# Kernel optimization log

Measured on AMD Instinct MI355X. Metric: run time of the kernel, lower is better.

## Reference

```python
import jax, jax.numpy as jnp
import numpy as np

N_NODES = 50000
N_EDGES = 800000
D = 128
DEPTH = 3


def setup_inputs() -> dict:
    key = jax.random.key(0)
    ks = jax.random.split(key, 10)
    s = 1.0 / np.sqrt(D)
    return {
        "h": jax.random.normal(ks[0], (N_NODES, D), dtype=jnp.float32),
        "src": jax.random.randint(ks[1], (N_EDGES,), 0, N_NODES, dtype=jnp.int32),
        "dst": jax.random.randint(ks[2], (N_EDGES,), 0, N_NODES, dtype=jnp.int32),
        "W_in1": jax.random.normal(ks[3], (D, D), dtype=jnp.float32) * s,
        "b_in1": jnp.zeros((D,), dtype=jnp.float32),
        "W_in2": jax.random.normal(ks[4], (D, D), dtype=jnp.float32) * s,
        "b_in2": jnp.zeros((D,), dtype=jnp.float32),
        "W_self": jax.random.normal(ks[5], (DEPTH, D, D), dtype=jnp.float32) * s,
        "b_self": jnp.zeros((DEPTH, D), dtype=jnp.float32),
        "W_neigh": jax.random.normal(ks[6], (DEPTH, D, D), dtype=jnp.float32) * s,
    }


def _mean_aggregate(h, src, dst, n_nodes):
    # gather source features along edges, sum into destination, divide by in-degree
    msg = h[src]                                             # [E, D]
    summed = jax.ops.segment_sum(msg, dst, num_segments=n_nodes)  # [N, D]
    deg = jax.ops.segment_sum(jnp.ones_like(dst, dtype=h.dtype), dst,
                              num_segments=n_nodes)          # [N]
    return summed / jnp.maximum(deg, 1.0)[:, None]


def reference(h, src, dst, W_in1, b_in1, W_in2, b_in2, W_self, b_self, W_neigh):
    n_nodes = h.shape[0]
    # fc_in: Linear -> tanh -> Linear
    h = jnp.tanh(h @ W_in1 + b_in1) @ W_in2 + b_in2
    # stacked SAGEConv(mean) layers with SiLU between layers
    for i in range(DEPTH):
        h_neigh = _mean_aggregate(h, src, dst, n_nodes)
        h = h @ W_self[i] + b_self[i] + h_neigh @ W_neigh[i]
        if i < DEPTH - 1:
            h = jax.nn.silu(h)
    return jnp.tanh(h)
```

## Files before the change

kernel.cpp:

```cpp
#include <hip/hip_runtime.h>
#include <stdint.h>

#define DD 128
#define LDSROW 136

typedef __attribute__((ext_vector_type(8))) short short8;
typedef __attribute__((ext_vector_type(4))) float float4v;

__device__ __forceinline__ unsigned short f2bf(float f) {
  unsigned u = __float_as_uint(f);
  unsigned r = u + 0x7fffu + ((u >> 16) & 1u);
  return (unsigned short)(r >> 16);
}
__device__ __forceinline__ unsigned pack2(float a, float b) {
  return (unsigned)f2bf(a) | ((unsigned)f2bf(b) << 16);
}
__device__ __forceinline__ float2 unpack2(unsigned p) {
  float2 r;
  r.x = __uint_as_float(p << 16);
  r.y = __uint_as_float(p & 0xffff0000u);
  return r;
}

__global__ __launch_bounds__(256) void k_deg_prep(const int* __restrict__ dst, int* deg, int e, int eb,
                                                  const float* __restrict__ W1, const float* __restrict__ W2,
                                                  const float* __restrict__ Wself, const float* __restrict__ Wneigh,
                                                  unsigned* __restrict__ wfrag) {
  int b = blockIdx.x;
  if (b < eb) {
    int i = b * 256 + threadIdx.x;
    if (i < e) atomicAdd(&deg[dst[i]], 1);
  } else {
    int gid = (b - eb) * 256 + threadIdx.x;
    int m = gid >> 13;
    int r = gid & 8191;
    int p = r & 3;
    int lane = (r >> 2) & 63;
    int t = (r >> 8) & 3;
    int c = r >> 10;
    const float* W;
    if (m == 0) W = W1;
    else if (m == 1) W = W2;
    else if (m < 5) W = Wself + (size_t)(m - 2) * DD * DD;
    else W = Wneigh + (size_t)(m - 5) * DD * DD;
    int n = c * 16 + (lane & 15);
    int k = t * 32 + (lane >> 4) * 8 + 2 * p;
    wfrag[gid] = pack2(W[(size_t)k * DD + n], W[(size_t)(k + 1) * DD + n]);
  }
}

__global__ __launch_bounds__(1024) void k_scan1(const int* __restrict__ deg, int* __restrict__ incl,
                                                int* __restrict__ bsum, int n) {
  __shared__ int sh[1024];
  int t = threadIdx.x;
  int i = blockIdx.x * 1024 + t;
  int v = (i < n) ? deg[i] : 0;
  sh[t] = v;
  __syncthreads();
#pragma unroll
  for (int off = 1; off < 1024; off <<= 1) {
    int add = (t >= off) ? sh[t - off] : 0;
    __syncthreads();
    sh[t] += add;
    __syncthreads();
  }
  if (i < n) incl[i] = sh[t];
  if (t == 1023) bsum[blockIdx.x] = sh[1023];
}

__global__ __launch_bounds__(1024) void k_scan3(const int* __restrict__ deg, const int* __restrict__ incl,
                                                const int* __restrict__ bsum, int* __restrict__ rowstart,
                                                int* __restrict__ cursor, int n, int nb) {
  __shared__ int sboff;
  int t = threadIdx.x;
  if (t < 64) {
    int orig = (t < nb) ? bsum[t] : 0;
    int v = orig;
#pragma unroll
    for (int off = 1; off < 64; off <<= 1) {
      int u = __shfl_up(v, off);
      if (t >= off) v += u;
    }
    if (t == (int)blockIdx.x) sboff = v - orig;
  }
  __syncthreads();
  int i = blockIdx.x * 1024 + t;
  if (i >= n) return;
  int d = deg[i];
  int excl = sboff + incl[i] - d;
  rowstart[i] = excl;
  cursor[i] = excl;
  if (i == n - 1) rowstart[n] = excl + d;
}

__global__ __launch_bounds__(512) void k_fill_r(const int* __restrict__ src, const int* __restrict__ dst,
                                                int* cursor, int* __restrict__ esrc, int e, int rstep) {
  int range = blockIdx.x & 7;
  int i = (blockIdx.x >> 3) * 512 + threadIdx.x;
  if (i >= e) return;
  int d = dst[i];
  int lo = range * rstep;
  if (d >= lo && d < lo + rstep) {
    int p = atomicAdd(&cursor[d], 1);
    esrc[p] = src[i];
  }
}

__global__ __launch_bounds__(256) void k_aggr(const uint4* __restrict__ h, const int* __restrict__ rowstart,
                                              const int* __restrict__ esrc, uint4* __restrict__ out, int n) {
  int wave = threadIdx.x >> 6, lane = threadIdx.x & 63;
  int g = lane >> 4, nn = lane & 15;
  int r = blockIdx.x * 4 + wave;
  if (r >= n) return;
  int ru = __builtin_amdgcn_readfirstlane(r);
  int beg = rowstart[ru], end = rowstart[ru + 1];
  int cnt = end - beg;
  float acc[8];
#pragma unroll
  for (int i = 0; i < 8; ++i) acc[i] = 0.f;
  int base = 0;
  for (; base + 16 <= cnt; base += 16) {
    int j0 = beg + base + g;
    int s0 = esrc[j0];
    int s1 = esrc[j0 + 4];
    int s2 = esrc[j0 + 8];
    int s3 = esrc[j0 + 12];
    uint4 v0 = h[(size_t)s0 * 16 + nn];
    uint4 v1 = h[(size_t)s1 * 16 + nn];
    uint4 v2 = h[(size_t)s2 * 16 + nn];
    uint4 v3 = h[(size_t)s3 * 16 + nn];
    const unsigned* u0 = (const unsigned*)&v0;
    const unsigned* u1 = (const unsigned*)&v1;
    const unsigned* u2 = (const unsigned*)&v2;
    const unsigned* u3 = (const unsigned*)&v3;
#pragma unroll
    for (int k = 0; k < 4; ++k) {
      float2 f0 = unpack2(u0[k]), f1 = unpack2(u1[k]);
      float2 f2 = unpack2(u2[k]), f3 = unpack2(u3[k]);
      acc[2 * k]     += (f0.x + f1.x) + (f2.x + f3.x);
      acc[2 * k + 1] += (f0.y + f1.y) + (f2.y + f3.y);
    }
  }
  for (; base + 8 <= cnt; base += 8) {
    int j0 = beg + base + g;
    int s0 = esrc[j0];
    int s1 = esrc[j0 + 4];
    uint4 v0 = h[(size_t)s0 * 16 + nn];
    uint4 v1 = h[(size_t)s1 * 16 + nn];
    const unsigned* u0 = (const unsigned*)&v0;
    const unsigned* u1 = (const unsigned*)&v1;
#pragma unroll
    for (int k = 0; k < 4; ++k) {
      float2 f0 = unpack2(u0[k]), f1 = unpack2(u1[k]);
      acc[2 * k] += f0.x + f1.x;
      acc[2 * k + 1] += f0.y + f1.y;
    }
  }
  if (base + g < cnt) {
    int s = esrc[beg + base + g];
    uint4 v = h[(size_t)s * 16 + nn];
    const unsigned* u = (const unsigned*)&v;
#pragma unroll
    for (int k = 0; k < 4; ++k) {
      float2 f = unpack2(u[k]);
      acc[2 * k] += f.x;
      acc[2 * k + 1] += f.y;
    }
  }
  if (base + 4 + g < cnt) {
    int s = esrc[beg + base + 4 + g];
    uint4 v = h[(size_t)s * 16 + nn];
    const unsigned* u = (const unsigned*)&v;
#pragma unroll
    for (int k = 0; k < 4; ++k) {
      float2 f = unpack2(u[k]);
      acc[2 * k] += f.x;
      acc[2 * k + 1] += f.y;
    }
  }
#pragma unroll
  for (int k = 0; k < 8; ++k) {
    acc[k] += __shfl_xor(acc[k], 16, 64);
    acc[k] += __shfl_xor(acc[k], 32, 64);
  }
  if (g == 0) {
    float inv = 1.0f / (float)(cnt > 1 ? cnt : 1);
    uint4 o;
    o.x = pack2(acc[0] * inv, acc[1] * inv);
    o.y = pack2(acc[2] * inv, acc[3] * inv);
    o.z = pack2(acc[4] * inv, acc[5] * inv);
    o.w = pack2(acc[6] * inv, acc[7] * inv);
    out[(size_t)r * 16 + nn] = o;
  }
}

__global__ __launch_bounds__(256) void k_fc12(const float* __restrict__ h,
                                              const uint4* __restrict__ wf1, const uint4* __restrict__ wf2,
                                              const float* __restrict__ b1, const float* __restrict__ b2,
                                              unsigned short* __restrict__ outbf, int n) {
  __shared__ unsigned short sT[64 * LDSROW];
  int tid = threadIdx.x, w = tid >> 6, lane = tid & 63;
  int q = lane >> 4, nn = lane & 15;
  int r0 = (blockIdx.x * 4 + w) * 16;
  int rr = r0 + nn; if (rr >= n) rr = n - 1;
  short8 a[4];
  {
    const float* X = h + (size_t)rr * DD;
#pragma unroll
    for (int t = 0; t < 4; ++t) {
      int k0 = t * 32 + q * 8;
      float4 f0 = *(const float4*)&X[k0];
      float4 f1 = *(const float4*)&X[k0 + 4];
      uint4 u;
      u.x = pack2(f0.x, f0.y); u.y = pack2(f0.z, f0.w);
      u.z = pack2(f1.x, f1.y); u.w = pack2(f1.z, f1.w);
      a[t] = __builtin_bit_cast(short8, u);
    }
  }
  float4v acc[8];
#pragma unroll
  for (int c = 0; c < 8; ++c) acc[c] = (float4v){0.f, 0.f, 0.f, 0.f};
#pragma unroll
  for (int c = 0; c < 8; ++c) {
#pragma unroll
    for (int t = 0; t < 4; ++t) {
      short8 b = __builtin_bit_cast(short8, wf1[(c * 4 + t) * 64 + lane]);
      acc[c] = __builtin_amdgcn_mfma_f32_16x16x32_bf16(a[t], b, acc[c], 0, 0, 0);
    }
  }
#pragma unroll
  for (int c = 0; c < 8; ++c) {
    float bc = b1[c * 16 + nn];
#pragma unroll
    for (int g = 0; g < 4; ++g) {
      int lr = w * 16 + q * 4 + g;
      sT[lr * LDSROW + c * 16 + nn] = f2bf(tanhf(acc[c][g] + bc));
    }
  }
  __syncthreads();
  short8 a2[4];
#pragma unroll
  for (int t = 0; t < 4; ++t) {
    const uint4* p = (const uint4*)&sT[(w * 16 + nn) * LDSROW + (t * 4 + q) * 8];
    a2[t] = __builtin_bit_cast(short8, *p);
  }
  float4v acc2[8];
#pragma unroll
  for (int c = 0; c < 8; ++c) acc2[c] = (float4v){0.f, 0.f, 0.f, 0.f};
#pragma unroll
  for (int c = 0; c < 8; ++c) {
#pragma unroll
    for (int t = 0; t < 4; ++t) {
      short8 b = __builtin_bit_cast(short8, wf2[(c * 4 + t) * 64 + lane]);
      acc2[c] = __builtin_amdgcn_mfma_f32_16x16x32_bf16(a2[t], b, acc2[c], 0, 0, 0);
    }
  }
#pragma unroll
  for (int c = 0; c < 8; ++c) {
    float bc = b2[c * 16 + nn];
#pragma unroll
    for (int g = 0; g < 4; ++g) {
      int row = r0 + q * 4 + g;
      if (row < n) outbf[(size_t)row * DD + c * 16 + nn] = f2bf(acc2[c][g] + bc);
    }
  }
}

template <int ACT, bool OUTF32>
__global__ __launch_bounds__(256) void k_sage(const uint4* __restrict__ X, const uint4* __restrict__ G,
                                              const uint4* __restrict__ wfs, const uint4* __restrict__ wfn,
                                              const float* __restrict__ bias, void* __restrict__ outp, int n) {
  int tid = threadIdx.x, w = tid >> 6, lane = tid & 63;
  int q = lane >> 4, nn = lane & 15;
  int r0 = (blockIdx.x * 4 + w) * 16;
  int rr = r0 + nn; if (rr >= n) rr = n - 1;
  short8 a[4], g[4];
  {
    const uint4* Xr = X + (size_t)rr * 16;
    const uint4* Gr = G + (size_t)rr * 16;
#pragma unroll
    for (int t = 0; t < 4; ++t) {
      a[t] = __builtin_bit_cast(short8, Xr[t * 4 + q]);
      g[t] = __builtin_bit_cast(short8, Gr[t * 4 + q]);
    }
  }
  float4v acc[8];
#pragma unroll
  for (int c = 0; c < 8; ++c) acc[c] = (float4v){0.f, 0.f, 0.f, 0.f};
#pragma unroll
  for (int c = 0; c < 8; ++c) {
#pragma unroll
    for (int t = 0; t < 4; ++t) {
      short8 b = __builtin_bit_cast(short8, wfs[(c * 4 + t) * 64 + lane]);
      acc[c] = __builtin_amdgcn_mfma_f32_16x16x32_bf16(a[t], b, acc[c], 0, 0, 0);
    }
#pragma unroll
    for (int t = 0; t < 4; ++t) {
      short8 b = __builtin_bit_cast(short8, wfn[(c * 4 + t) * 64 + lane]);
      acc[c] = __builtin_amdgcn_mfma_f32_16x16x32_bf16(g[t], b, acc[c], 0, 0, 0);
    }
  }
#pragma unroll
  for (int c = 0; c < 8; ++c) {
    float bc = bias[c * 16 + nn];
#pragma unroll
    for (int gg = 0; gg < 4; ++gg) {
      int row = r0 + q * 4 + gg;
      if (row < n) {
        float v = acc[c][gg] + bc;
        if (ACT == 1) v = tanhf(v);
        else v = v / (1.f + __expf(-v));
        if (OUTF32) ((float*)outp)[(size_t)row * DD + c * 16 + nn] = v;
        else ((unsigned short*)outp)[(size_t)row * DD + c * 16 + nn] = f2bf(v);
      }
    }
  }
}

extern "C" void kernel_launch(void* const* d_in, const int* in_sizes, int n_in,
                              void* d_out, int out_size, void* d_ws, size_t ws_size,
                              hipStream_t stream) {
  const float* h_in = (const float*)d_in[0];
  const int* src    = (const int*)d_in[1];
  const int* dst    = (const int*)d_in[2];
  const float* W1   = (const float*)d_in[3];
  const float* b1   = (const float*)d_in[4];
  const float* W2   = (const float*)d_in[5];
  const float* b2   = (const float*)d_in[6];
  const float* Wself  = (const float*)d_in[7];
  const float* bself  = (const float*)d_in[8];
  const float* Wneigh = (const float*)d_in[9];
  const int N = in_sizes[0] / DD;
  const int E = in_sizes[1];
  float* out = (float*)d_out;

  char* ws = (char*)d_ws;
  size_t off = 0;
  auto alloc = [&](size_t bytes) -> char* {
    char* p = ws + off;
    off = (off + bytes + 255) & ~(size_t)255;
    return p;
  };
  unsigned* wfrag = (unsigned*)alloc(8 * 32768);
  unsigned* actA  = (unsigned*)alloc((size_t)N * 64 * 4);
  unsigned* actB  = (unsigned*)alloc((size_t)N * 64 * 4);
  unsigned* neigh = (unsigned*)alloc((size_t)N * 64 * 4);
  int* esrc     = (int*)alloc((size_t)E * 4);
  int* degi     = (int*)alloc((size_t)N * 4);
  int* rowstart = (int*)alloc((size_t)(N + 1) * 4);
  int* cursor   = (int*)alloc((size_t)N * 4);
  int* incl     = (int*)alloc((size_t)N * 4);
  int* bsum     = (int*)alloc(65 * 4);

  hipMemsetAsync(degi, 0, (size_t)N * 4, stream);
  const int eb = (E + 255) / 256;
  const int eb5 = (E + 511) / 512;
  const int nb = (N + 1023) / 1024;
  const int rstep = (N + 7) / 8;
  k_deg_prep<<<eb + 256, 256, 0, stream>>>(dst, degi, E, eb, W1, W2, Wself, Wneigh, wfrag);
  k_scan1<<<nb, 1024, 0, stream>>>(degi, incl, bsum, N);
  k_scan3<<<nb, 1024, 0, stream>>>(degi, incl, bsum, rowstart, cursor, N, nb);
  k_fill_r<<<eb5 * 8, 512, 0, stream>>>(src, dst, cursor, esrc, E, rstep);

  const int gb = (N + 63) / 64;
  const int ab = (N + 3) / 4;
  const uint4* wf = (const uint4*)wfrag;

  k_fc12<<<gb, 256, 0, stream>>>(h_in, wf + 0 * 2048, wf + 1 * 2048, b1, b2,
                                 (unsigned short*)actB, N);

  const unsigned* cur = actB;
  unsigned* nxt = actA;
  for (int l = 0; l < 3; ++l) {
    k_aggr<<<ab, 256, 0, stream>>>((const uint4*)cur, rowstart, esrc, (uint4*)neigh, N);
    const uint4* wsF = wf + (size_t)(2 + l) * 2048;
    const uint4* wnF = wf + (size_t)(5 + l) * 2048;
    const float* bs = bself + (size_t)l * DD;
    if (l < 2) {
      k_sage<2, false><<<gb, 256, 0, stream>>>((const uint4*)cur, (const uint4*)neigh, wsF, wnF, bs, nxt, N);
      const unsigned* tmp = cur;
      cur = nxt;
      nxt = (unsigned*)tmp;
    } else {
      k_sage<1, true><<<gb, 256, 0, stream>>>((const uint4*)cur, (const uint4*)neigh, wsF, wnF, bs, out, N);
    }
  }
}
```

Before: 335.0 us.

## Fuse mean aggregation into SAGE layer kernel via LDS staging

Merges the separate gather/mean aggregation kernel into the per-layer MFMA kernel. Each block aggregates neighbors for its 64 rows, writes bf16 means to shared memory, then feeds them straight into the neighbor matmul. This removes the neigh buffer round trip through global memory and one launch per layer. In exchange, aggregation now uses 16 lanes per row with a serial loop over edges instead of 64 lanes, which reduces memory-level parallelism and raises the chance of load imbalance from degree variance across the 4 rows each lane group handles.

```diff
diff --git a/kernel.cpp b/kernel.cpp
--- a/kernel.cpp
+++ b/kernel.cpp
@@ -106,94 +106,6 @@
   }
 }
 
-__global__ __launch_bounds__(256) void k_aggr(const uint4* __restrict__ h, const int* __restrict__ rowstart,
-                                              const int* __restrict__ esrc, uint4* __restrict__ out, int n) {
-  int wave = threadIdx.x >> 6, lane = threadIdx.x & 63;
-  int g = lane >> 4, nn = lane & 15;
-  int r = blockIdx.x * 4 + wave;
-  if (r >= n) return;
-  int ru = __builtin_amdgcn_readfirstlane(r);
-  int beg = rowstart[ru], end = rowstart[ru + 1];
-  int cnt = end - beg;
-  float acc[8];
-#pragma unroll
-  for (int i = 0; i < 8; ++i) acc[i] = 0.f;
-  int base = 0;
-  for (; base + 16 <= cnt; base += 16) {
-    int j0 = beg + base + g;
-    int s0 = esrc[j0];
-    int s1 = esrc[j0 + 4];
-    int s2 = esrc[j0 + 8];
-    int s3 = esrc[j0 + 12];
-    uint4 v0 = h[(size_t)s0 * 16 + nn];
-    uint4 v1 = h[(size_t)s1 * 16 + nn];
-    uint4 v2 = h[(size_t)s2 * 16 + nn];
-    uint4 v3 = h[(size_t)s3 * 16 + nn];
-    const unsigned* u0 = (const unsigned*)&v0;
-    const unsigned* u1 = (const unsigned*)&v1;
-    const unsigned* u2 = (const unsigned*)&v2;
-    const unsigned* u3 = (const unsigned*)&v3;
-#pragma unroll
-    for (int k = 0; k < 4; ++k) {
-      float2 f0 = unpack2(u0[k]), f1 = unpack2(u1[k]);
-      float2 f2 = unpack2(u2[k]), f3 = unpack2(u3[k]);
-      acc[2 * k]     += (f0.x + f1.x) + (f2.x + f3.x);
-      acc[2 * k + 1] += (f0.y + f1.y) + (f2.y + f3.y);
-    }
-  }
-  for (; base + 8 <= cnt; base += 8) {
-    int j0 = beg + base + g;
-    int s0 = esrc[j0];
-    int s1 = esrc[j0 + 4];
-    uint4 v0 = h[(size_t)s0 * 16 + nn];
-    uint4 v1 = h[(size_t)s1 * 16 + nn];
-    const unsigned* u0 = (const unsigned*)&v0;
-    const unsigned* u1 = (const unsigned*)&v1;
-#pragma unroll
-    for (int k = 0; k < 4; ++k) {
-      float2 f0 = unpack2(u0[k]), f1 = unpack2(u1[k]);
-      acc[2 * k] += f0.x + f1.x;
-      acc[2 * k + 1] += f0.y + f1.y;
-    }
-  }
-  if (base + g < cnt) {
-    int s = esrc[beg + base + g];
-    uint4 v = h[(size_t)s * 16 + nn];
-    const unsigned* u = (const unsigned*)&v;
-#pragma unroll
-    for (int k = 0; k < 4; ++k) {
-      float2 f = unpack2(u[k]);
-      acc[2 * k] += f.x;
-      acc[2 * k + 1] += f.y;
-    }
-  }
-  if (base + 4 + g < cnt) {
-    int s = esrc[beg + base + 4 + g];
-    uint4 v = h[(size_t)s * 16 + nn];
-    const unsigned* u = (const unsigned*)&v;
-#pragma unroll
-    for (int k = 0; k < 4; ++k) {
-      float2 f = unpack2(u[k]);
-      acc[2 * k] += f.x;
-      acc[2 * k + 1] += f.y;
-    }
-  }
-#pragma unroll
-  for (int k = 0; k < 8; ++k) {
-    acc[k] += __shfl_xor(acc[k], 16, 64);
-    acc[k] += __shfl_xor(acc[k], 32, 64);
-  }
-  if (g == 0) {
-    float inv = 1.0f / (float)(cnt > 1 ? cnt : 1);
-    uint4 o;
-    o.x = pack2(acc[0] * inv, acc[1] * inv);
-    o.y = pack2(acc[2] * inv, acc[3] * inv);
-    o.z = pack2(acc[4] * inv, acc[5] * inv);
-    o.w = pack2(acc[6] * inv, acc[7] * inv);
-    out[(size_t)r * 16 + nn] = o;
-  }
-}
-
 __global__ __launch_bounds__(256) void k_fc12(const float* __restrict__ h,
                                               const uint4* __restrict__ wf1, const uint4* __restrict__ wf2,
                                               const float* __restrict__ b1, const float* __restrict__ b2,
@@ -267,21 +179,104 @@
 }
 
 template <int ACT, bool OUTF32>
-__global__ __launch_bounds__(256) void k_sage(const uint4* __restrict__ X, const uint4* __restrict__ G,
-                                              const uint4* __restrict__ wfs, const uint4* __restrict__ wfn,
-                                              const float* __restrict__ bias, void* __restrict__ outp, int n) {
+__global__ __launch_bounds__(256) void k_layer(const uint4* __restrict__ X,
+                                               const int* __restrict__ rowstart, const int* __restrict__ esrc,
+                                               const uint4* __restrict__ wfs, const uint4* __restrict__ wfn,
+                                               const float* __restrict__ bias, void* __restrict__ outp, int n) {
+  __shared__ unsigned short sG[64 * LDSROW];
   int tid = threadIdx.x, w = tid >> 6, lane = tid & 63;
   int q = lane >> 4, nn = lane & 15;
-  int r0 = (blockIdx.x * 4 + w) * 16;
-  int rr = r0 + nn; if (rr >= n) rr = n - 1;
-  short8 a[4], g[4];
+  int r0 = blockIdx.x * 64;
+  for (int j = 0; j < 4; ++j) {
+    int lr = w * 16 + q * 4 + j;
+    int r = r0 + lr;
+    if (r < n) {
+      int beg = rowstart[r];
+      int cnt = rowstart[r + 1] - beg;
+      float acc[8];
+#pragma unroll
+      for (int i = 0; i < 8; ++i) acc[i] = 0.f;
+      int base = 0;
+      for (; base + 8 <= cnt; base += 8) {
+        int j0 = beg + base;
+        int s0 = esrc[j0], s1 = esrc[j0 + 1], s2 = esrc[j0 + 2], s3 = esrc[j0 + 3];
+        int s4 = esrc[j0 + 4], s5 = esrc[j0 + 5], s6 = esrc[j0 + 6], s7 = esrc[j0 + 7];
+        uint4 v0 = X[(size_t)s0 * 16 + nn];
+        uint4 v1 = X[(size_t)s1 * 16 + nn];
+        uint4 v2 = X[(size_t)s2 * 16 + nn];
+        uint4 v3 = X[(size_t)s3 * 16 + nn];
+        uint4 v4 = X[(size_t)s4 * 16 + nn];
+        uint4 v5 = X[(size_t)s5 * 16 + nn];
+        uint4 v6 = X[(size_t)s6 * 16 + nn];
+        uint4 v7 = X[(size_t)s7 * 16 + nn];
+        const unsigned* u0 = (const unsigned*)&v0;
+        const unsigned* u1 = (const unsigned*)&v1;
+        const unsigned* u2 = (const unsigned*)&v2;
+        const unsigned* u3 = (const unsigned*)&v3;
+        const unsigned* u4 = (const unsigned*)&v4;
+        const unsigned* u5 = (const unsigned*)&v5;
+        const unsigned* u6 = (const unsigned*)&v6;
+        const unsigned* u7 = (const unsigned*)&v7;
+#pragma unroll
+        for (int k = 0; k < 4; ++k) {
+          float2 f0 = unpack2(u0[k]), f1 = unpack2(u1[k]);
+          float2 f2 = unpack2(u2[k]), f3 = unpack2(u3[k]);
+          float2 f4 = unpack2(u4[k]), f5 = unpack2(u5[k]);
+          float2 f6 = unpack2(u6[k]), f7 = unpack2(u7[k]);
+          acc[2 * k]     += ((f0.x + f1.x) + (f2.x + f3.x)) + ((f4.x + f5.x) + (f6.x + f7.x));
+          acc[2 * k + 1] += ((f0.y + f1.y) + (f2.y + f3.y)) + ((f4.y + f5.y) + (f6.y + f7.y));
+        }
+      }
+      if (base + 4 <= cnt) {
+        int j0 = beg + base;
+        int s0 = esrc[j0], s1 = esrc[j0 + 1], s2 = esrc[j0 + 2], s3 = esrc[j0 + 3];
+        uint4 v0 = X[(size_t)s0 * 16 + nn];
+        uint4 v1 = X[(size_t)s1 * 16 + nn];
+        uint4 v2 = X[(size_t)s2 * 16 + nn];
+        uint4 v3 = X[(size_t)s3 * 16 + nn];
+        const unsigned* u0 = (const unsigned*)&v0;
+        const unsigned* u1 = (const unsigned*)&v1;
+        const unsigned* u2 = (const unsigned*)&v2;
+        const unsigned* u3 = (const unsigned*)&v3;
+#pragma unroll
+        for (int k = 0; k < 4; ++k) {
+          float2 f0 = unpack2(u0[k]), f1 = unpack2(u1[k]);
+          float2 f2 = unpack2(u2[k]), f3 = unpack2(u3[k]);
+          acc[2 * k]     += (f0.x + f1.x) + (f2.x + f3.x);
+          acc[2 * k + 1] += (f0.y + f1.y) + (f2.y + f3.y);
+        }
+        base += 4;
+      }
+      for (; base < cnt; ++base) {
+        int s = esrc[beg + base];
+        uint4 v = X[(size_t)s * 16 + nn];
+        const unsigned* u = (const unsigned*)&v;
+#pragma unroll
+        for (int k = 0; k < 4; ++k) {
+          float2 f = unpack2(u[k]);
+          acc[2 * k] += f.x;
+          acc[2 * k + 1] += f.y;
+        }
+      }
+      float inv = 1.0f / (float)(cnt > 1 ? cnt : 1);
+      uint4 o;
+      o.x = pack2(acc[0] * inv, acc[1] * inv);
+      o.y = pack2(acc[2] * inv, acc[3] * inv);
+      o.z = pack2(acc[4] * inv, acc[5] * inv);
+      o.w = pack2(acc[6] * inv, acc[7] * inv);
+      *(uint4*)&sG[lr * LDSROW + nn * 8] = o;
+    }
+  }
+  __syncthreads();
+  int r0w = r0 + w * 16;
+  int rr = r0w + nn; if (rr >= n) rr = n - 1;
+  short8 a[4], gf[4];
   {
     const uint4* Xr = X + (size_t)rr * 16;
-    const uint4* Gr = G + (size_t)rr * 16;
 #pragma unroll
     for (int t = 0; t < 4; ++t) {
       a[t] = __builtin_bit_cast(short8, Xr[t * 4 + q]);
-      g[t] = __builtin_bit_cast(short8, Gr[t * 4 + q]);
+      gf[t] = __builtin_bit_cast(short8, *(const uint4*)&sG[(w * 16 + nn) * LDSROW + (t * 4 + q) * 8]);
     }
   }
   float4v acc[8];
@@ -297,7 +292,7 @@
 #pragma unroll
     for (int t = 0; t < 4; ++t) {
       short8 b = __builtin_bit_cast(short8, wfn[(c * 4 + t) * 64 + lane]);
-      acc[c] = __builtin_amdgcn_mfma_f32_16x16x32_bf16(g[t], b, acc[c], 0, 0, 0);
+      acc[c] = __builtin_amdgcn_mfma_f32_16x16x32_bf16(gf[t], b, acc[c], 0, 0, 0);
     }
   }
 #pragma unroll
@@ -305,7 +300,7 @@
     float bc = bias[c * 16 + nn];
 #pragma unroll
     for (int gg = 0; gg < 4; ++gg) {
-      int row = r0 + q * 4 + gg;
+      int row = r0w + q * 4 + gg;
       if (row < n) {
         float v = acc[c][gg] + bc;
         if (ACT == 1) v = tanhf(v);
@@ -344,7 +339,6 @@
   unsigned* wfrag = (unsigned*)alloc(8 * 32768);
   unsigned* actA  = (unsigned*)alloc((size_t)N * 64 * 4);
   unsigned* actB  = (unsigned*)alloc((size_t)N * 64 * 4);
-  unsigned* neigh = (unsigned*)alloc((size_t)N * 64 * 4);
   int* esrc     = (int*)alloc((size_t)E * 4);
   int* degi     = (int*)alloc((size_t)N * 4);
   int* rowstart = (int*)alloc((size_t)(N + 1) * 4);
@@ -363,7 +357,6 @@
   k_fill_r<<<eb5 * 8, 512, 0, stream>>>(src, dst, cursor, esrc, E, rstep);
 
   const int gb = (N + 63) / 64;
-  const int ab = (N + 3) / 4;
   const uint4* wf = (const uint4*)wfrag;
 
   k_fc12<<<gb, 256, 0, stream>>>(h_in, wf + 0 * 2048, wf + 1 * 2048, b1, b2,
@@ -372,17 +365,16 @@
   const unsigned* cur = actB;
   unsigned* nxt = actA;
   for (int l = 0; l < 3; ++l) {
-    k_aggr<<<ab, 256, 0, stream>>>((const uint4*)cur, rowstart, esrc, (uint4*)neigh, N);
     const uint4* wsF = wf + (size_t)(2 + l) * 2048;
     const uint4* wnF = wf + (size_t)(5 + l) * 2048;
     const float* bs = bself + (size_t)l * DD;
     if (l < 2) {
-      k_sage<2, false><<<gb, 256, 0, stream>>>((const uint4*)cur, (const uint4*)neigh, wsF, wnF, bs, nxt, N);
+      k_layer<2, false><<<gb, 256, 0, stream>>>((const uint4*)cur, rowstart, esrc, wsF, wnF, bs, nxt, N);
       const unsigned* tmp = cur;
       cur = nxt;
       nxt = (unsigned*)tmp;
     } else {
-      k_sage<1, true><<<gb, 256, 0, stream>>>((const uint4*)cur, (const uint4*)neigh, wsF, wnF, bs, out, N);
-    }
-  }
-}
+      k_layer<1, true><<<gb, 256, 0, stream>>>((const uint4*)cur, rowstart, esrc, wsF, wnF, bs, out, N);
+    }
+  }
+}
```

Measured after the change: 390.2 us. +16.5%, slower.
